# Performance work log

Measured on AMD Instinct MI355X. Metric: run time of the kernel, lower is better.

## Reference

```python
import jax, jax.numpy as jnp
import numpy as np

B, T, S, H = 32, 512, 1024, 1024

def setup_inputs() -> dict:
    key = jax.random.key(0)
    k1, k2, k3, k4, k5, k6 = jax.random.split(key, 6)
    query = jax.random.normal(k1, (B, T, H), dtype=jnp.float32)
    encoder_outputs = jax.random.normal(k2, (B, S, H), dtype=jnp.float32)
    # lengths in [S//2, S], force max length == S so mask width matches score
    src_lengths = jax.random.randint(k3, (B,), S // 2, S + 1, dtype=jnp.int32)
    src_lengths = src_lengths.at[0].set(S).astype(jnp.int64)
    scale = 1.0 / np.sqrt(H)
    W_in = jax.random.normal(k4, (H, H), dtype=jnp.float32) * scale      # linear_in.weight
    W_out = jax.random.normal(k5, (H, 2 * H), dtype=jnp.float32) * scale # linear_out.weight
    b_out = jax.random.normal(k6, (H,), dtype=jnp.float32) * scale       # linear_out.bias
    return {"query": query, "encoder_outputs": encoder_outputs,
            "src_lengths": src_lengths, "W_in": W_in, "W_out": W_out, "b_out": b_out}

def reference(query, encoder_outputs, src_lengths, W_in, W_out, b_out):
    # padding mask: True where position >= length  [B, S]
    pad = jnp.arange(S)[None, :] >= src_lengths[:, None]
    # linear_in (no bias): [B, T, H]
    qw = jnp.einsum('bth,oh->bto', query, W_in)
    # scores: [B, T, S]
    score = jnp.einsum('bto,bso->bts', qw, encoder_outputs)
    score = jnp.where(pad[:, None, :], -jnp.inf, score)
    p = jax.nn.softmax(score, axis=2)
    # context: [B, T, H]
    c = jnp.einsum('bts,bsh->bth', p, encoder_outputs)
    concat = jnp.concatenate([query, c], axis=2)          # [B, T, 2H]
    out = jnp.tanh(jnp.einsum('btk,ok->bto', concat, W_out) + b_out)
    return out
```

## Files before the change

kernel.cpp:

```cpp
#include <hip/hip_runtime.h>
#include <math.h>

#define BB 32
#define TT 512
#define SS 1024
#define HH 1024

typedef __attribute__((ext_vector_type(8))) short short8;
typedef __attribute__((ext_vector_type(4))) float f32x4;
typedef __attribute__((ext_vector_type(4))) unsigned short u16x4;
typedef unsigned short u16;

__device__ __forceinline__ u16 f2h(float x) {
    union { float f; unsigned int u; } a; a.f = x;
    unsigned int u = a.u;
    return (u16)((u + 0x7fffu + ((u >> 16) & 1u)) >> 16);
}
__device__ __forceinline__ float h2f(u16 h) {
    union { unsigned int u; float f; } a; a.u = ((unsigned int)h) << 16;
    return a.f;
}

__device__ __forceinline__ void gll16(const u16* g, u16* l) {
    __builtin_amdgcn_global_load_lds(
        (const __attribute__((address_space(1))) void*)g,
        (__attribute__((address_space(3))) void*)l, 16, 0, 0);
}

enum { E_F32 = 0, E_SPLIT = 1, E_TANH = 2, E_H = 3 };

struct Segs { const u16* a[4]; const u16* b[4]; };

template<int NSEG, int EPI>
__global__ __launch_bounds__(512, 2) void gemm8(
    Segs sg, int ldA, int ldB, int zshift,
    long sA, long sB, long sC,
    const float* __restrict__ bias,
    float* __restrict__ Cf, u16* __restrict__ Ch, u16* __restrict__ Cl,
    int ldC)
{
    __shared__ u16 lds[2][2][2][256 * 32];

    const int tid = threadIdx.x;
    const int l = tid & 63, w = tid >> 6;
    const int wr = w >> 2, wc = w & 3;
    const int fr = l & 15, g = l >> 4;

    const int id = blockIdx.x;
    const int v = ((id & 7) << 5) | (id >> 3);
    const int z = v >> zshift;
    const int rest = v & ((1 << zshift) - 1);
    const int bm = (rest >> 2) * 256;
    const int bn = (rest & 3) * 256;

    const u16* Aseg[4]; const u16* Bseg[4];
#pragma unroll
    for (int s = 0; s < NSEG; ++s) {
        Aseg[s] = sg.a[s] + (long)z * sA;
        Bseg[s] = sg.b[s] + (long)z * sB;
    }
    if (EPI == E_F32 || EPI == E_TANH) Cf += (long)z * sC;
    else { Ch += (long)z * sC; if (EPI == E_SPLIT) Cl += (long)z * sC; }

    f32x4 acc[8][4] = {};

    const int srow = tid >> 2, sch = tid & 3;
    const int skc = sch ^ ((srow >> 1) & 3);
    const long grA0 = (long)(bm + srow) * ldA + skc * 8;
    const long grA1 = (long)(bm + 128 + srow) * ldA + skc * 8;
    const long grB0 = (long)(bn + srow) * ldB + skc * 8;
    const long grB1 = (long)(bn + 128 + srow) * ldB + skc * 8;
    const int ldst0 = (tid & ~63) * 8;
    const int ldst1 = (512 + (tid & ~63)) * 8;

    auto stage = [&](int tile, int kh, int tensor) {
        const int k0g = tile * 64 + kh * 32;
        const int seg = k0g >> 10, kl = k0g & 1023;
        u16* lb = &lds[tile & 1][tensor][kh][0];
        if (tensor) {
            const u16* b = Bseg[seg];
            gll16(b + grB0 + kl, lb + ldst0);
            gll16(b + grB1 + kl, lb + ldst1);
        } else {
            const u16* a = Aseg[seg];
            gll16(a + grA0 + kl, lb + ldst0);
            gll16(a + grA1 + kl, lb + ldst1);
        }
    };

    int offA[8], offB[4];
#pragma unroll
    for (int k = 0; k < 8; ++k) {
        const int r = wr * 128 + k * 16 + fr;
        offA[k] = (r * 4 + (g ^ ((r >> 1) & 3))) * 8;
    }
#pragma unroll
    for (int j = 0; j < 4; ++j) {
        const int r = wc * 64 + j * 16 + fr;
        offB[j] = (r * 4 + (g ^ ((r >> 1) & 3))) * 8;
    }

    short8 faX[4], faY[4], fbA[4], fbB[4];

#define PFA(FA, BUF, KS, MH)                                                   \
    { const u16* pl = &lds[BUF][0][KS][0];                                     \
      _Pragma("unroll") for (int i_ = 0; i_ < 4; ++i_)                         \
          FA[i_] = *(const short8*)&pl[offA[(MH) * 4 + i_]]; }
#define PFB(FB, BUF, KS)                                                       \
    { const u16* pl = &lds[BUF][1][KS][0];                                     \
      _Pragma("unroll") for (int j_ = 0; j_ < 4; ++j_)                         \
          FB[j_] = *(const short8*)&pl[offB[j_]]; }
#define MFMA16(FA, FB, MH)                                                     \
    __builtin_amdgcn_s_setprio(1);                                             \
    _Pragma("unroll") for (int i_ = 0; i_ < 4; ++i_)                           \
        _Pragma("unroll") for (int j_ = 0; j_ < 4; ++j_)                       \
            acc[(MH) * 4 + i_][j_] = __builtin_amdgcn_mfma_f32_16x16x32_bf16(  \
                FA[i_], FB[j_], acc[(MH) * 4 + i_][j_], 0, 0, 0);              \
    __builtin_amdgcn_s_setprio(0);

    stage(0, 0, 0); stage(0, 0, 1); stage(0, 1, 0); stage(0, 1, 1);
    asm volatile("s_waitcnt vmcnt(0)" ::: "memory");
    __builtin_amdgcn_s_barrier();
    PFB(fbA, 0, 0)
    PFA(faX, 0, 0, 0)
    __builtin_amdgcn_sched_barrier(0);

    const int NT = NSEG * 16;
    for (int t = 0; t < NT; ++t) {
        const int cur = t & 1, nxt = cur ^ 1;
        const bool nl = (t + 1 < NT);
        if (nl) stage(t + 1, 0, 0);
        __builtin_amdgcn_s_barrier();
        PFA(faY, cur, 0, 1)
        __builtin_amdgcn_sched_barrier(0);
        MFMA16(faX, fbA, 1)
        ;
        break;
    }

#pragma unroll
    for (int i = 0; i < 8; ++i)
#pragma unroll
        for (int j = 0; j < 4; ++j) acc[i][j] = f32x4{0.f, 0.f, 0.f, 0.f};
    __builtin_amdgcn_s_barrier();
    stage(0, 0, 0); stage(0, 0, 1); stage(0, 1, 0); stage(0, 1, 1);
    asm volatile("s_waitcnt vmcnt(0)" ::: "memory");
    __builtin_amdgcn_s_barrier();
    PFB(fbA, 0, 0)
    PFA(faX, 0, 0, 0)
    __builtin_amdgcn_sched_barrier(0);

    for (int t = 0; t < NT; ++t) {
        const int cur = t & 1, nxt = cur ^ 1;
        const bool nl = (t + 1 < NT);

        if (nl) stage(t + 1, 0, 0);
        __builtin_amdgcn_s_barrier();
        PFA(faY, cur, 0, 1)
        __builtin_amdgcn_sched_barrier(0);
        MFMA16(faX, fbA, 0)

        if (nl) stage(t + 1, 0, 1);
        if (nl) { asm volatile("s_waitcnt vmcnt(4)" ::: "memory"); }
        else    { asm volatile("s_waitcnt vmcnt(0)" ::: "memory"); }
        __builtin_amdgcn_s_barrier();
        PFB(fbB, cur, 1)
        PFA(faX, cur, 1, 0)
        __builtin_amdgcn_sched_barrier(0);
        MFMA16(faY, fbA, 1)

        if (nl) stage(t + 1, 1, 0);
        __builtin_amdgcn_s_barrier();
        PFA(faY, cur, 1, 1)
        __builtin_amdgcn_sched_barrier(0);
        MFMA16(faX, fbB, 0)

        if (nl) stage(t + 1, 1, 1);
        if (nl) { asm volatile("s_waitcnt vmcnt(4)" ::: "memory"); }
        __builtin_amdgcn_s_barrier();
        PFB(fbA, nxt, 0)
        PFA(faX, nxt, 0, 0)
        __builtin_amdgcn_sched_barrier(0);
        MFMA16(faY, fbB, 1)
    }
#undef PFA
#undef PFB
#undef MFMA16

#pragma unroll
    for (int mi = 0; mi < 8; ++mi) {
        const int row0 = bm + wr * 128 + mi * 16 + g * 4;
#pragma unroll
        for (int nj = 0; nj < 4; ++nj) {
            const int col = bn + wc * 64 + nj * 16 + fr;
            const float bv = (EPI == E_TANH) ? bias[col] : 0.0f;
#pragma unroll
            for (int r = 0; r < 4; ++r) {
                const float vv = acc[mi][nj][r];
                const long o = (long)(row0 + r) * ldC + col;
                if (EPI == E_TANH) {
                    const float e = __expf(2.0f * (vv + bv));
                    Cf[o] = 1.0f - 2.0f / (e + 1.0f);
                } else if (EPI == E_F32) {
                    Cf[o] = vv;
                } else if (EPI == E_SPLIT) {
                    const u16 h = f2h(vv);
                    Ch[o] = h; Cl[o] = f2h(vv - h2f(h));
                } else {
                    Ch[o] = f2h(vv);
                }
            }
        }
    }
}

__global__ __launch_bounds__(256) void split_f32(
    const float* __restrict__ in, u16* __restrict__ hi, u16* __restrict__ lo,
    long n4)
{
    long i = (long)blockIdx.x * blockDim.x + threadIdx.x;
    const long stride = (long)gridDim.x * blockDim.x;
    for (; i < n4; i += stride) {
        f32x4 v = *(const f32x4*)(in + i * 4);
        u16x4 h4, l4;
#pragma unroll
        for (int e = 0; e < 4; ++e) {
            u16 h_ = f2h(v[e]);
            h4[e] = h_; l4[e] = f2h(v[e] - h2f(h_));
        }
        *(u16x4*)(hi + i * 4) = h4;
        *(u16x4*)(lo + i * 4) = l4;
    }
}

__global__ __launch_bounds__(256) void transpose_h(
    const float* __restrict__ in, u16* __restrict__ out)
{
    __shared__ float t[64][65];
    const int z = blockIdx.z, sb = blockIdx.x * 64, hb = blockIdx.y * 64;
    const int c4 = (threadIdx.x & 15) * 4, r0 = threadIdx.x >> 4;
    const float* src = in + ((long)z * SS + sb) * HH + hb;
#pragma unroll
    for (int i = 0; i < 4; ++i) {
        const int r = r0 + i * 16;
        f32x4 v = *(const f32x4*)(src + (long)r * HH + c4);
        t[c4 + 0][r] = v.x; t[c4 + 1][r] = v.y;
        t[c4 + 2][r] = v.z; t[c4 + 3][r] = v.w;
    }
    __syncthreads();
    u16* dst = out + ((long)z * HH + hb) * SS + sb;
#pragma unroll
    for (int i = 0; i < 4; ++i) {
        const int r = r0 + i * 16;
        u16x4 o;
#pragma unroll
        for (int j = 0; j < 4; ++j) o[j] = f2h(t[r][c4 + j]);
        *(u16x4*)(dst + (long)r * SS + c4) = o;
    }
}

__global__ __launch_bounds__(256) void softmax_mask(
    const float* __restrict__ Sc, u16* __restrict__ Ph,
    const int* __restrict__ lens)
{
    const int row = blockIdx.x;
    const int b = row >> 9;
    const int len = lens[b];
    const float* p = Sc + (long)row * SS;

    const int tid = threadIdx.x;
    const int s0 = tid * 4;
    f32x4 v = *(const f32x4*)(p + s0);
    float vals[4] = {v.x, v.y, v.z, v.w};

    float mx = -INFINITY;
#pragma unroll
    for (int j = 0; j < 4; ++j) {
        if (s0 + j >= len) vals[j] = -INFINITY;
        mx = fmaxf(mx, vals[j]);
    }
    for (int off = 32; off; off >>= 1) mx = fmaxf(mx, __shfl_xor(mx, off, 64));

    __shared__ float redm[4];
    __shared__ float reds[4];
    const int wave = tid >> 6, lane = tid & 63;
    if (lane == 0) redm[wave] = mx;
    __syncthreads();
    mx = fmaxf(fmaxf(redm[0], redm[1]), fmaxf(redm[2], redm[3]));

    float sum = 0.0f;
#pragma unroll
    for (int j = 0; j < 4; ++j) {
        vals[j] = __expf(vals[j] - mx);
        sum += vals[j];
    }
    for (int off = 32; off; off >>= 1) sum += __shfl_xor(sum, off, 64);
    if (lane == 0) reds[wave] = sum;
    __syncthreads();
    sum = reds[0] + reds[1] + reds[2] + reds[3];

    const float inv = 1.0f / sum;
    u16x4 o;
#pragma unroll
    for (int j = 0; j < 4; ++j) o[j] = f2h(vals[j] * inv);
    *(u16x4*)(Ph + (long)row * SS + s0) = o;
}

extern "C" void kernel_launch(void* const* d_in, const int* in_sizes, int n_in,
                              void* d_out, int out_size, void* d_ws, size_t ws_size,
                              hipStream_t stream)
{
    const float* query = (const float*)d_in[0];
    const float* enc   = (const float*)d_in[1];
    const int*   lens  = (const int*)d_in[2];
    const float* W_in  = (const float*)d_in[3];
    const float* W_out = (const float*)d_in[4];
    const float* b_out = (const float*)d_in[5];
    float* out = (float*)d_out;

    const long MQ = (long)BB * TT;

    u16* qh   = (u16*)d_ws;
    u16* ql   = qh   + MQ * HH;
    u16* qwh  = ql   + MQ * HH;
    u16* qwl  = qwh  + MQ * HH;
    u16* ench = qwl  + MQ * HH;
    u16* encl = ench + (long)BB * SS * HH;
    u16* ph   = encl + (long)BB * SS * HH;
    u16* wih  = ph   + MQ * SS;
    u16* wil  = wih  + (long)HH * HH;
    u16* woh  = wil  + (long)HH * HH;
    u16* wol  = woh  + (long)HH * 2 * HH;
    float* scores = (float*)(wol + (long)HH * 2 * HH);
    u16* encTh = (u16*)scores;
    u16* ch   = ql;

    split_f32<<<2048, 256, 0, stream>>>(query, qh, ql, MQ * HH / 4);
    split_f32<<<512, 256, 0, stream>>>(W_in, wih, wil, (long)HH * HH / 4);
    split_f32<<<512, 256, 0, stream>>>(W_out, woh, wol, (long)HH * 2 * HH / 4);
    split_f32<<<2048, 256, 0, stream>>>(enc, ench, encl, (long)BB * SS * HH / 4);

    Segs s1 = {{qh, qh, ql, nullptr}, {wih, wil, wih, nullptr}};
    gemm8<3, E_SPLIT><<<256, 512, 0, stream>>>(
        s1, HH, HH, 8, 0L, 0L, 0L, nullptr, nullptr, qwh, qwl, HH);

    Segs s2 = {{qwh, qwh, qwl, nullptr}, {ench, encl, ench, nullptr}};
    gemm8<3, E_F32><<<256, 512, 0, stream>>>(
        s2, HH, HH, 3, (long)TT * HH, (long)SS * HH, (long)TT * SS,
        nullptr, scores, nullptr, nullptr, SS);

    softmax_mask<<<BB * TT, 256, 0, stream>>>(scores, ph, lens);

    transpose_h<<<dim3(16, 16, 32), 256, 0, stream>>>(enc, encTh);

    Segs s3 = {{ph, nullptr, nullptr, nullptr}, {encTh, nullptr, nullptr, nullptr}};
    gemm8<1, E_H><<<256, 512, 0, stream>>>(
        s3, SS, SS, 3, (long)TT * SS, (long)HH * SS, (long)TT * HH,
        nullptr, nullptr, ch, nullptr, HH);

    Segs s4 = {{qh, ch, qh, ch},
               {woh, woh + 1024, wol, wol + 1024}};
    gemm8<4, E_TANH><<<256, 512, 0, stream>>>(
        s4, HH, 2 * HH, 8, 0L, 0L, 0L, b_out, out, nullptr, nullptr, HH);
}
```

Baseline: 498.3 us.

## Replace 256x256 8-wave GEMM with 256x128 4-wave double-buffered kernel

Swaps the 512-thread 256x256 output tile GEMM for a 256-thread 256x128 tile with a single-stage K=32 double-buffered pipeline and a simpler per-iteration barrier scheme. It also removes the odd warm-up pass that ran one iteration, zeroed the accumulators and re-staged. The grid doubles to 512 blocks with adjusted z-shifts and block swizzle. This trades lower per-block data reuse and an extra barrier per iteration for more blocks, simpler scheduling and less LDS per block.

```diff
diff --git a/kernel.cpp b/kernel.cpp
--- a/kernel.cpp
+++ b/kernel.cpp
@@ -32,26 +32,27 @@
 struct Segs { const u16* a[4]; const u16* b[4]; };
 
 template<int NSEG, int EPI>
-__global__ __launch_bounds__(512, 2) void gemm8(
+__global__ __launch_bounds__(256, 2) void gemm2p(
     Segs sg, int ldA, int ldB, int zshift,
     long sA, long sB, long sC,
     const float* __restrict__ bias,
     float* __restrict__ Cf, u16* __restrict__ Ch, u16* __restrict__ Cl,
     int ldC)
 {
-    __shared__ u16 lds[2][2][2][256 * 32];
+    __shared__ u16 Abuf[2][256 * 32];
+    __shared__ u16 Bbuf[2][128 * 32];
 
     const int tid = threadIdx.x;
     const int l = tid & 63, w = tid >> 6;
-    const int wr = w >> 2, wc = w & 3;
+    const int wr = w >> 1, wc = w & 1;
     const int fr = l & 15, g = l >> 4;
 
     const int id = blockIdx.x;
-    const int v = ((id & 7) << 5) | (id >> 3);
+    const int v = (id & 7) * 64 + (id >> 3);
     const int z = v >> zshift;
     const int rest = v & ((1 << zshift) - 1);
-    const int bm = (rest >> 2) * 256;
-    const int bn = (rest & 3) * 256;
+    const int bm = (rest >> 3) * 256;
+    const int bn = (rest & 7) * 128;
 
     const u16* Aseg[4]; const u16* Bseg[4];
 #pragma unroll
@@ -66,26 +67,26 @@
 
     const int srow = tid >> 2, sch = tid & 3;
     const int skc = sch ^ ((srow >> 1) & 3);
-    const long grA0 = (long)(bm + srow) * ldA + skc * 8;
-    const long grA1 = (long)(bm + 128 + srow) * ldA + skc * 8;
-    const long grB0 = (long)(bn + srow) * ldB + skc * 8;
-    const long grB1 = (long)(bn + 128 + srow) * ldB + skc * 8;
-    const int ldst0 = (tid & ~63) * 8;
-    const int ldst1 = (512 + (tid & ~63)) * 8;
-
-    auto stage = [&](int tile, int kh, int tensor) {
-        const int k0g = tile * 64 + kh * 32;
+    long grA[4], grB[2];
+#pragma unroll
+    for (int r = 0; r < 4; ++r) grA[r] = (long)(bm + r * 64 + srow) * ldA + skc * 8;
+#pragma unroll
+    for (int r = 0; r < 2; ++r) grB[r] = (long)(bn + r * 64 + srow) * ldB + skc * 8;
+    const int wub = tid & ~63;
+
+    auto stage = [&](int tile) {
+        const int k0g = tile * 32;
         const int seg = k0g >> 10, kl = k0g & 1023;
-        u16* lb = &lds[tile & 1][tensor][kh][0];
-        if (tensor) {
-            const u16* b = Bseg[seg];
-            gll16(b + grB0 + kl, lb + ldst0);
-            gll16(b + grB1 + kl, lb + ldst1);
-        } else {
-            const u16* a = Aseg[seg];
-            gll16(a + grA0 + kl, lb + ldst0);
-            gll16(a + grA1 + kl, lb + ldst1);
-        }
+        const u16* a = Aseg[seg];
+        u16* la = &Abuf[tile & 1][0];
+#pragma unroll
+        for (int r = 0; r < 4; ++r)
+            gll16(a + grA[r] + kl, la + ((r * 256 + wub) << 3));
+        const u16* b = Bseg[seg];
+        u16* lb = &Bbuf[tile & 1][0];
+#pragma unroll
+        for (int r = 0; r < 2; ++r)
+            gll16(b + grB[r] + kl, lb + ((r * 256 + wub) << 3));
     };
 
     int offA[8], offB[4];
@@ -100,16 +101,6 @@
         offB[j] = (r * 4 + (g ^ ((r >> 1) & 3))) * 8;
     }
 
-    short8 faX[4], faY[4], fbA[4], fbB[4];
-
-#define PFA(FA, BUF, KS, MH)                                                   \
-    { const u16* pl = &lds[BUF][0][KS][0];                                     \
-      _Pragma("unroll") for (int i_ = 0; i_ < 4; ++i_)                         \
-          FA[i_] = *(const short8*)&pl[offA[(MH) * 4 + i_]]; }
-#define PFB(FB, BUF, KS)                                                       \
-    { const u16* pl = &lds[BUF][1][KS][0];                                     \
-      _Pragma("unroll") for (int j_ = 0; j_ < 4; ++j_)                         \
-          FB[j_] = *(const short8*)&pl[offB[j_]]; }
 #define MFMA16(FA, FB, MH)                                                     \
     __builtin_amdgcn_s_setprio(1);                                             \
     _Pragma("unroll") for (int i_ = 0; i_ < 4; ++i_)                           \
@@ -118,73 +109,44 @@
                 FA[i_], FB[j_], acc[(MH) * 4 + i_][j_], 0, 0, 0);              \
     __builtin_amdgcn_s_setprio(0);
 
-    stage(0, 0, 0); stage(0, 0, 1); stage(0, 1, 0); stage(0, 1, 1);
+    stage(0);
     asm volatile("s_waitcnt vmcnt(0)" ::: "memory");
     __builtin_amdgcn_s_barrier();
-    PFB(fbA, 0, 0)
-    PFA(faX, 0, 0, 0)
-    __builtin_amdgcn_sched_barrier(0);
-
-    const int NT = NSEG * 16;
+    asm volatile("" ::: "memory");
+
+    const int NT = NSEG * 32;
     for (int t = 0; t < NT; ++t) {
-        const int cur = t & 1, nxt = cur ^ 1;
+        const int cur = t & 1;
         const bool nl = (t + 1 < NT);
-        if (nl) stage(t + 1, 0, 0);
+        const u16* Ap = &Abuf[cur][0];
+        const u16* Bp = &Bbuf[cur][0];
+
+        if (nl) {
+            stage(t + 1);
+            asm volatile("s_waitcnt vmcnt(6)" ::: "memory");
+        } else {
+            asm volatile("s_waitcnt vmcnt(0)" ::: "memory");
+        }
         __builtin_amdgcn_s_barrier();
-        PFA(faY, cur, 0, 1)
+        asm volatile("" ::: "memory");
+
+        short8 fb[4], fa[4];
+#pragma unroll
+        for (int j = 0; j < 4; ++j) fb[j] = *(const short8*)&Bp[offB[j]];
+#pragma unroll
+        for (int i = 0; i < 4; ++i) fa[i] = *(const short8*)&Ap[offA[i]];
         __builtin_amdgcn_sched_barrier(0);
-        MFMA16(faX, fbA, 1)
-        ;
-        break;
-    }
-
-#pragma unroll
-    for (int i = 0; i < 8; ++i)
-#pragma unroll
-        for (int j = 0; j < 4; ++j) acc[i][j] = f32x4{0.f, 0.f, 0.f, 0.f};
-    __builtin_amdgcn_s_barrier();
-    stage(0, 0, 0); stage(0, 0, 1); stage(0, 1, 0); stage(0, 1, 1);
-    asm volatile("s_waitcnt vmcnt(0)" ::: "memory");
-    __builtin_amdgcn_s_barrier();
-    PFB(fbA, 0, 0)
-    PFA(faX, 0, 0, 0)
-    __builtin_amdgcn_sched_barrier(0);
-
-    for (int t = 0; t < NT; ++t) {
-        const int cur = t & 1, nxt = cur ^ 1;
-        const bool nl = (t + 1 < NT);
-
-        if (nl) stage(t + 1, 0, 0);
+        MFMA16(fa, fb, 0)
+
+#pragma unroll
+        for (int i = 0; i < 4; ++i) fa[i] = *(const short8*)&Ap[offA[4 + i]];
+        __builtin_amdgcn_sched_barrier(0);
+        MFMA16(fa, fb, 1)
+
+        asm volatile("s_waitcnt lgkmcnt(0)" ::: "memory");
         __builtin_amdgcn_s_barrier();
-        PFA(faY, cur, 0, 1)
-        __builtin_amdgcn_sched_barrier(0);
-        MFMA16(faX, fbA, 0)
-
-        if (nl) stage(t + 1, 0, 1);
-        if (nl) { asm volatile("s_waitcnt vmcnt(4)" ::: "memory"); }
-        else    { asm volatile("s_waitcnt vmcnt(0)" ::: "memory"); }
-        __builtin_amdgcn_s_barrier();
-        PFB(fbB, cur, 1)
-        PFA(faX, cur, 1, 0)
-        __builtin_amdgcn_sched_barrier(0);
-        MFMA16(faY, fbA, 1)
-
-        if (nl) stage(t + 1, 1, 0);
-        __builtin_amdgcn_s_barrier();
-        PFA(faY, cur, 1, 1)
-        __builtin_amdgcn_sched_barrier(0);
-        MFMA16(faX, fbB, 0)
-
-        if (nl) stage(t + 1, 1, 1);
-        if (nl) { asm volatile("s_waitcnt vmcnt(4)" ::: "memory"); }
-        __builtin_amdgcn_s_barrier();
-        PFB(fbA, nxt, 0)
-        PFA(faX, nxt, 0, 0)
-        __builtin_amdgcn_sched_barrier(0);
-        MFMA16(faY, fbB, 1)
-    }
-#undef PFA
-#undef PFB
+        asm volatile("" ::: "memory");
+    }
 #undef MFMA16
 
 #pragma unroll
@@ -341,12 +303,12 @@
     split_f32<<<2048, 256, 0, stream>>>(enc, ench, encl, (long)BB * SS * HH / 4);
 
     Segs s1 = {{qh, qh, ql, nullptr}, {wih, wil, wih, nullptr}};
-    gemm8<3, E_SPLIT><<<256, 512, 0, stream>>>(
-        s1, HH, HH, 8, 0L, 0L, 0L, nullptr, nullptr, qwh, qwl, HH);
+    gemm2p<3, E_SPLIT><<<512, 256, 0, stream>>>(
+        s1, HH, HH, 9, 0L, 0L, 0L, nullptr, nullptr, qwh, qwl, HH);
 
     Segs s2 = {{qwh, qwh, qwl, nullptr}, {ench, encl, ench, nullptr}};
-    gemm8<3, E_F32><<<256, 512, 0, stream>>>(
-        s2, HH, HH, 3, (long)TT * HH, (long)SS * HH, (long)TT * SS,
+    gemm2p<3, E_F32><<<512, 256, 0, stream>>>(
+        s2, HH, HH, 4, (long)TT * HH, (long)SS * HH, (long)TT * SS,
         nullptr, scores, nullptr, nullptr, SS);
 
     softmax_mask<<<BB * TT, 256, 0, stream>>>(scores, ph, lens);
@@ -354,12 +316,12 @@
     transpose_h<<<dim3(16, 16, 32), 256, 0, stream>>>(enc, encTh);
 
     Segs s3 = {{ph, nullptr, nullptr, nullptr}, {encTh, nullptr, nullptr, nullptr}};
-    gemm8<1, E_H><<<256, 512, 0, stream>>>(
-        s3, SS, SS, 3, (long)TT * SS, (long)HH * SS, (long)TT * HH,
+    gemm2p<1, E_H><<<512, 256, 0, stream>>>(
+        s3, SS, SS, 4, (long)TT * SS, (long)HH * SS, (long)TT * HH,
         nullptr, nullptr, ch, nullptr, HH);
 
     Segs s4 = {{qh, ch, qh, ch},
                {woh, woh + 1024, wol, wol + 1024}};
-    gemm8<4, E_TANH><<<256, 512, 0, stream>>>(
-        s4, HH, 2 * HH, 8, 0L, 0L, 0L, b_out, out, nullptr, nullptr, HH);
-}
+    gemm2p<4, E_TANH><<<512, 256, 0, stream>>>(
+        s4, HH, 2 * HH, 9, 0L, 0L, 0L, b_out, out, nullptr, nullptr, HH);
+}
```

New measurement: 583.3 us. 1.17x slower.

## Replace double-buffered fragment pipeline with single-buffer synchronized MFMA phases

Applied to the files above, without the earlier changes.

Drops the ping-pong A/B fragment registers and the stray warmup iteration that re-staged the first tile, and instead loads fragments just before each MFMA group, guarded by a barrier and a full LDS wait. This reduces register use and the redundant prologue work, but serializes LDS reads with matrix math and adds extra barriers per k-step.

```diff
diff --git a/kernel.cpp b/kernel.cpp
--- a/kernel.cpp
+++ b/kernel.cpp
@@ -100,92 +100,61 @@
         offB[j] = (r * 4 + (g ^ ((r >> 1) & 3))) * 8;
     }
 
-    short8 faX[4], faY[4], fbA[4], fbB[4];
-
-#define PFA(FA, BUF, KS, MH)                                                   \
+    short8 fa[4], fb[4];
+
+#define PFA(BUF, KS, MH)                                                       \
     { const u16* pl = &lds[BUF][0][KS][0];                                     \
       _Pragma("unroll") for (int i_ = 0; i_ < 4; ++i_)                         \
-          FA[i_] = *(const short8*)&pl[offA[(MH) * 4 + i_]]; }
-#define PFB(FB, BUF, KS)                                                       \
+          fa[i_] = *(const short8*)&pl[offA[(MH) * 4 + i_]]; }
+#define PFB(BUF, KS)                                                           \
     { const u16* pl = &lds[BUF][1][KS][0];                                     \
       _Pragma("unroll") for (int j_ = 0; j_ < 4; ++j_)                         \
-          FB[j_] = *(const short8*)&pl[offB[j_]]; }
-#define MFMA16(FA, FB, MH)                                                     \
+          fb[j_] = *(const short8*)&pl[offB[j_]]; }
+#define SYNC_MFMA(MH)                                                          \
+    __builtin_amdgcn_s_barrier();                                              \
+    asm volatile("s_waitcnt lgkmcnt(0)" ::: "memory");                         \
+    __builtin_amdgcn_sched_barrier(0);                                         \
     __builtin_amdgcn_s_setprio(1);                                             \
     _Pragma("unroll") for (int i_ = 0; i_ < 4; ++i_)                           \
         _Pragma("unroll") for (int j_ = 0; j_ < 4; ++j_)                       \
             acc[(MH) * 4 + i_][j_] = __builtin_amdgcn_mfma_f32_16x16x32_bf16(  \
-                FA[i_], FB[j_], acc[(MH) * 4 + i_][j_], 0, 0, 0);              \
-    __builtin_amdgcn_s_setprio(0);
+                fa[i_], fb[j_], acc[(MH) * 4 + i_][j_], 0, 0, 0);              \
+    __builtin_amdgcn_s_setprio(0);                                             \
+    __builtin_amdgcn_s_barrier();
 
     stage(0, 0, 0); stage(0, 0, 1); stage(0, 1, 0); stage(0, 1, 1);
     asm volatile("s_waitcnt vmcnt(0)" ::: "memory");
     __builtin_amdgcn_s_barrier();
-    PFB(fbA, 0, 0)
-    PFA(faX, 0, 0, 0)
-    __builtin_amdgcn_sched_barrier(0);
 
     const int NT = NSEG * 16;
     for (int t = 0; t < NT; ++t) {
-        const int cur = t & 1, nxt = cur ^ 1;
+        const int cur = t & 1;
         const bool nl = (t + 1 < NT);
+
+        PFB(cur, 0)
+        PFA(cur, 0, 0)
         if (nl) stage(t + 1, 0, 0);
-        __builtin_amdgcn_s_barrier();
-        PFA(faY, cur, 0, 1)
-        __builtin_amdgcn_sched_barrier(0);
-        MFMA16(faX, fbA, 1)
-        ;
-        break;
-    }
-
-#pragma unroll
-    for (int i = 0; i < 8; ++i)
-#pragma unroll
-        for (int j = 0; j < 4; ++j) acc[i][j] = f32x4{0.f, 0.f, 0.f, 0.f};
-    __builtin_amdgcn_s_barrier();
-    stage(0, 0, 0); stage(0, 0, 1); stage(0, 1, 0); stage(0, 1, 1);
-    asm volatile("s_waitcnt vmcnt(0)" ::: "memory");
-    __builtin_amdgcn_s_barrier();
-    PFB(fbA, 0, 0)
-    PFA(faX, 0, 0, 0)
-    __builtin_amdgcn_sched_barrier(0);
-
-    for (int t = 0; t < NT; ++t) {
-        const int cur = t & 1, nxt = cur ^ 1;
-        const bool nl = (t + 1 < NT);
-
-        if (nl) stage(t + 1, 0, 0);
-        __builtin_amdgcn_s_barrier();
-        PFA(faY, cur, 0, 1)
-        __builtin_amdgcn_sched_barrier(0);
-        MFMA16(faX, fbA, 0)
-
-        if (nl) stage(t + 1, 0, 1);
-        if (nl) { asm volatile("s_waitcnt vmcnt(4)" ::: "memory"); }
+        SYNC_MFMA(0)
+
+        PFA(cur, 0, 1)
+        if (nl) { stage(t + 1, 0, 1);
+                  asm volatile("s_waitcnt vmcnt(4)" ::: "memory"); }
         else    { asm volatile("s_waitcnt vmcnt(0)" ::: "memory"); }
-        __builtin_amdgcn_s_barrier();
-        PFB(fbB, cur, 1)
-        PFA(faX, cur, 1, 0)
-        __builtin_amdgcn_sched_barrier(0);
-        MFMA16(faY, fbA, 1)
-
+        SYNC_MFMA(1)
+
+        PFB(cur, 1)
+        PFA(cur, 1, 0)
         if (nl) stage(t + 1, 1, 0);
-        __builtin_amdgcn_s_barrier();
-        PFA(faY, cur, 1, 1)
-        __builtin_amdgcn_sched_barrier(0);
-        MFMA16(faX, fbB, 0)
-
-        if (nl) stage(t + 1, 1, 1);
-        if (nl) { asm volatile("s_waitcnt vmcnt(4)" ::: "memory"); }
-        __builtin_amdgcn_s_barrier();
-        PFB(fbA, nxt, 0)
-        PFA(faX, nxt, 0, 0)
-        __builtin_amdgcn_sched_barrier(0);
-        MFMA16(faY, fbB, 1)
+        SYNC_MFMA(0)
+
+        PFA(cur, 1, 1)
+        if (nl) { stage(t + 1, 1, 1);
+                  asm volatile("s_waitcnt vmcnt(4)" ::: "memory"); }
+        SYNC_MFMA(1)
     }
 #undef PFA
 #undef PFB
-#undef MFMA16
+#undef SYNC_MFMA
 
 #pragma unroll
     for (int mi = 0; mi < 8; ++mi) {
```

Result: no change. 500.8 us (+0.5%).
